# Optimization experiments

Hardware: AMD Instinct MI355X
Metric: run time of the kernel (lower is better)

Reference implementation:

```python
import jax, jax.numpy as jnp
import numpy as np

DIM = 1024
NUM_HEADS = 16
HEAD_DIM = DIM // NUM_HEADS
SCALE = DIM ** (-0.5)  # NOTE: original scales by full dim, not head_dim


def setup_inputs() -> dict:
    key = jax.random.key(0)
    ks = jax.random.split(key, 5)
    B, S = 2, 2048
    x = jax.random.normal(ks[0], (B, S, DIM), dtype=jnp.float32)
    w_qkv = jax.random.normal(ks[1], (DIM, 3 * DIM), dtype=jnp.float32) * (DIM ** -0.5)
    b_qkv = jax.random.normal(ks[2], (3 * DIM,), dtype=jnp.float32) * 0.02
    w_proj = jax.random.normal(ks[3], (DIM, DIM), dtype=jnp.float32) * (DIM ** -0.5)
    b_proj = jax.random.normal(ks[4], (DIM,), dtype=jnp.float32) * 0.02
    return {"x": x, "w_qkv": w_qkv, "b_qkv": b_qkv, "w_proj": w_proj, "b_proj": b_proj}


def reference(x, w_qkv, b_qkv, w_proj, b_proj):
    B, S, D = x.shape
    qkv = x @ w_qkv + b_qkv                                  # [B,S,3D]
    qkv = qkv.reshape(B, S, NUM_HEADS, 3 * HEAD_DIM).transpose(0, 2, 1, 3)  # [B,H,S,3hd]
    q, k, v = jnp.split(qkv, 3, axis=-1)                     # each [B,H,S,hd]
    attn = jnp.einsum("bhqd,bhkd->bhqk", q, k) * SCALE       # [B,H,S,S]
    attn = jax.nn.softmax(attn, axis=-1)
    out = jnp.einsum("bhqk,bhkd->bhqd", attn, v)             # [B,H,S,hd]
    out = out.transpose(0, 2, 1, 3).reshape(B, S, D)
    return out @ w_proj + b_proj
```

## Files before the change

kernel.cpp:

```cpp
#include <hip/hip_runtime.h>
#include <hip/hip_bf16.h>

#define DIM 1024
#define NH 16
#define HD 64
#define BB 2
#define SS 2048
#define MROWS (BB * SS)
#define SCALE 0.03125f
#define SC_LOG2E 0.04508422002778011f

typedef unsigned short u16;
typedef unsigned int u32;
typedef __attribute__((ext_vector_type(8))) short short8;
typedef __attribute__((ext_vector_type(4))) float f32x4;

__device__ __forceinline__ u16 f2bf(float f) {
  union { float f; u32 u; } v; v.f = f;
  return (u16)((v.u + 0x7fffu + ((v.u >> 16) & 1u)) >> 16);
}

__device__ __forceinline__ u32 pack2bf(float a, float b) {
  union { __hip_bfloat162 h; u32 u; } cv;
  cv.h = __float22bfloat162_rn(make_float2(a, b));
  return cv.u;
}

__device__ __forceinline__ void async16(const u16* g, u16* l) {
  __builtin_amdgcn_global_load_lds(
      (const __attribute__((address_space(1))) void*)(const void*)g,
      (__attribute__((address_space(3))) void*)(void*)l, 16, 0, 0);
}

__device__ __forceinline__ short8 ld8(const u16* p) { return *(const short8*)p; }

__global__ void cvt_kernel(const float* __restrict__ in, u16* __restrict__ out, int n4) {
  int i = blockIdx.x * blockDim.x + threadIdx.x;
  if (i < n4) {
    float4 v = ((const float4*)in)[i];
    u32 lo = (u32)f2bf(v.x) | ((u32)f2bf(v.y) << 16);
    u32 hi = (u32)f2bf(v.z) | ((u32)f2bf(v.w) << 16);
    ((uint2*)out)[i] = make_uint2(lo, hi);
  }
}

__global__ void tconv_kernel(const float* __restrict__ in, u16* __restrict__ out, int R, int C) {
  __shared__ u16 t[64 * 65];
  int c0 = blockIdx.x * 64, r0 = blockIdx.y * 64;
  #pragma unroll
  for (int i = 0; i < 16; i++) {
    int j = i * 256 + threadIdx.x;
    int rr = j >> 6, cc = j & 63;
    t[rr * 65 + cc] = f2bf(in[(size_t)(r0 + rr) * C + c0 + cc]);
  }
  __syncthreads();
  #pragma unroll
  for (int i = 0; i < 16; i++) {
    int j = i * 256 + threadIdx.x;
    int oc = j >> 6, orr = j & 63;
    out[(size_t)(c0 + oc) * R + r0 + orr] = t[orr * 65 + oc];
  }
}

template <int MODE>
__global__ __launch_bounds__(256, 2) void gemm_bt(
    const u16* __restrict__ A, const u16* __restrict__ Bt,
    const float* __restrict__ bias, void* __restrict__ C,
    u16* __restrict__ vT, int M, int N, int K) {
  __shared__ __align__(16) u16 As[128 * 32];
  __shared__ __align__(16) u16 Bs[128 * 32];
  const int tid = threadIdx.x;
  const int w = tid >> 6, l = tid & 63;
  const int r = l & 15, q = l >> 4;
  const int m0 = blockIdx.y * 128, n0 = blockIdx.x * 128;
  const int qm = (w & 1) * 64, qn = (w >> 1) * 64;

  const size_t aoff = (size_t)(m0 + w * 16 + (l >> 2)) * K + (size_t)(l & 3) * 8;
  const size_t boff = (size_t)(n0 + w * 16 + (l >> 2)) * K + (size_t)(l & 3) * 8;
  u16* alds = &As[(w * 64 + l) * 8];
  u16* blds = &Bs[(w * 64 + l) * 8];

  f32x4 acc[4][4] = {};
  for (int k0 = 0; k0 < K; k0 += 32) {
    async16(A + aoff + k0, alds);
    async16(A + aoff + (size_t)64 * K + k0, alds + 2048);
    async16(Bt + boff + k0, blds);
    async16(Bt + boff + (size_t)64 * K + k0, blds + 2048);
    __syncthreads();
    short8 af[4], bfr[4];
    #pragma unroll
    for (int i = 0; i < 4; i++) af[i] = ld8(&As[(qm + i * 16 + r) * 32 + q * 8]);
    #pragma unroll
    for (int j = 0; j < 4; j++) bfr[j] = ld8(&Bs[(qn + j * 16 + r) * 32 + q * 8]);
    #pragma unroll
    for (int i = 0; i < 4; i++)
      #pragma unroll
      for (int j = 0; j < 4; j++)
        acc[i][j] = __builtin_amdgcn_mfma_f32_16x16x32_bf16(af[i], bfr[j], acc[i][j], 0, 0, 0);
    __syncthreads();
  }
  #pragma unroll
  for (int i = 0; i < 4; i++) {
    int ro = m0 + qm + i * 16 + q * 4;
    #pragma unroll
    for (int j = 0; j < 4; j++) {
      int col = n0 + qn + j * 16 + r;
      float bv = bias[col];
      float v0 = acc[i][j][0] + bv, v1 = acc[i][j][1] + bv;
      float v2 = acc[i][j][2] + bv, v3 = acc[i][j][3] + bv;
      if (MODE == 1) {
        float* out = (float*)C;
        out[(size_t)(ro + 0) * N + col] = v0;
        out[(size_t)(ro + 1) * N + col] = v1;
        out[(size_t)(ro + 2) * N + col] = v2;
        out[(size_t)(ro + 3) * N + col] = v3;
      } else {
        int h = col / 192, wi = col - h * 192;
        if (wi >= 128) {
          int bb = ro >> 11, s = ro & 2047, d = wi - 128;
          uint2 pk = make_uint2(pack2bf(v0, v1), pack2bf(v2, v3));
          *(uint2*)&vT[((size_t)((bb * NH + h) * HD + d)) * SS + s] = pk;
        } else {
          u16* qk2 = (u16*)C;
          qk2[(size_t)(ro + 0) * 2048 + h * 128 + wi] = f2bf(v0);
          qk2[(size_t)(ro + 1) * 2048 + h * 128 + wi] = f2bf(v1);
          qk2[(size_t)(ro + 2) * 2048 + h * 128 + wi] = f2bf(v2);
          qk2[(size_t)(ro + 3) * 2048 + h * 128 + wi] = f2bf(v3);
        }
      }
    }
  }
}

__global__ __launch_bounds__(256, 2) void attn3_kernel(
    const u16* __restrict__ qk2, const u16* __restrict__ vT,
    u16* __restrict__ attno) {
  __shared__ __align__(16) u16 Ks[128 * 64];
  __shared__ __align__(16) u16 Vs[64 * 128];
  __shared__ __align__(16) u16 pb[4][32 * 136];
  const int tid = threadIdx.x;
  const int w = tid >> 6, l = tid & 63;
  const int r = l & 15, q = l >> 4;
  const int b = blockIdx.z, h = blockIdx.y, q0 = blockIdx.x * 128;

  const u16* qb = qk2 + (size_t)b * SS * 2048;
  const u16* kB = qb + h * 128 + 64;
  const u16* vB = vT + (size_t)((b * NH + h) * HD) * SS;
  u16* pw = &pb[w][0];

  short8 qf[2][2];
  #pragma unroll
  for (int i = 0; i < 2; i++)
    #pragma unroll
    for (int kq = 0; kq < 2; kq++)
      qf[i][kq] = ld8(qb + (size_t)(q0 + w * 32 + i * 16 + r) * 2048 + h * 128 + kq * 32 + q * 8);

  const int klrow = l >> 3;
  const int kchunk = (l & 7) ^ klrow;
  const int vlrow = l >> 4;
  const int vslot = l & 15;

  f32x4 oacc[2][4] = {};
  float lacc[2] = {0.f, 0.f};

  for (int kv0 = 0; kv0 < SS; kv0 += 128) {
    #pragma unroll
    for (int t = 0; t < 4; t++) {
      int sl = (w * 4 + t) * 8 + klrow;
      async16(kB + (size_t)(kv0 + sl) * 2048 + kchunk * 8, &Ks[(w * 4 + t) * 512 + l * 8]);
    }
    #pragma unroll
    for (int t = 0; t < 4; t++) {
      int d = (w * 4 + t) * 4 + vlrow;
      int c = vslot ^ (t * 4 + vlrow);
      async16(vB + (size_t)d * SS + kv0 + c * 8, &Vs[(w * 4 + t) * 512 + l * 8]);
    }
    __syncthreads();

    f32x4 sacc[8][2] = {};
    #pragma unroll
    for (int j = 0; j < 8; j++) {
      int sl = j * 16 + r;
      short8 a0 = ld8(&Ks[sl * 64 + ((q ^ (r & 7)) * 8)]);
      short8 a1 = ld8(&Ks[sl * 64 + (((4 + q) ^ (r & 7)) * 8)]);
      #pragma unroll
      for (int i = 0; i < 2; i++) {
        sacc[j][i] = __builtin_amdgcn_mfma_f32_16x16x32_bf16(a0, qf[i][0], sacc[j][i], 0, 0, 0);
        sacc[j][i] = __builtin_amdgcn_mfma_f32_16x16x32_bf16(a1, qf[i][1], sacc[j][i], 0, 0, 0);
      }
    }
    float rs0 = 0.f, rs1 = 0.f;
    #pragma unroll
    for (int j = 0; j < 8; j++)
      #pragma unroll
      for (int i = 0; i < 2; i++) {
        float p0 = __builtin_exp2f(sacc[j][i][0] * SC_LOG2E);
        float p1 = __builtin_exp2f(sacc[j][i][1] * SC_LOG2E);
        float p2 = __builtin_exp2f(sacc[j][i][2] * SC_LOG2E);
        float p3 = __builtin_exp2f(sacc[j][i][3] * SC_LOG2E);
        if (i == 0) rs0 += (p0 + p1) + (p2 + p3);
        else        rs1 += (p0 + p1) + (p2 + p3);
        uint2 pk = make_uint2(pack2bf(p0, p1), pack2bf(p2, p3));
        *(uint2*)&pw[(i * 16 + r) * 136 + j * 16 + q * 4] = pk;
      }
    rs0 += __shfl_xor(rs0, 16); rs0 += __shfl_xor(rs0, 32);
    rs1 += __shfl_xor(rs1, 16); rs1 += __shfl_xor(rs1, 32);
    lacc[0] += rs0;
    lacc[1] += rs1;
    #pragma unroll
    for (int ks = 0; ks < 4; ks++) {
      short8 pa0 = ld8(&pw[(size_t)r * 136 + ks * 32 + q * 8]);
      short8 pa1 = ld8(&pw[(size_t)(16 + r) * 136 + ks * 32 + q * 8]);
      #pragma unroll
      for (int dj = 0; dj < 4; dj++) {
        short8 vb = ld8(&Vs[(dj * 16 + r) * 128 + (((ks * 4 + q) ^ r) * 8)]);
        oacc[0][dj] = __builtin_amdgcn_mfma_f32_16x16x32_bf16(pa0, vb, oacc[0][dj], 0, 0, 0);
        oacc[1][dj] = __builtin_amdgcn_mfma_f32_16x16x32_bf16(pa1, vb, oacc[1][dj], 0, 0, 0);
      }
    }
    __syncthreads();
  }
  #pragma unroll
  for (int i = 0; i < 2; i++)
    #pragma unroll
    for (int e = 0; e < 4; e++) {
      float dn = __shfl(lacc[i], q * 4 + e, 16);
      float di = 1.f / dn;
      int row = q0 + w * 32 + i * 16 + q * 4 + e;
      #pragma unroll
      for (int dj = 0; dj < 4; dj++)
        attno[(size_t)(b * SS + row) * DIM + h * HD + dj * 16 + r] =
            f2bf(oacc[i][dj][e] * di);
    }
}

extern "C" void kernel_launch(void* const* d_in, const int* in_sizes, int n_in,
                              void* d_out, int out_size, void* d_ws, size_t ws_size,
                              hipStream_t stream) {
  const float* x      = (const float*)d_in[0];
  const float* w_qkv  = (const float*)d_in[1];
  const float* b_qkv  = (const float*)d_in[2];
  const float* w_proj = (const float*)d_in[3];
  const float* b_proj = (const float*)d_in[4];
  float* out = (float*)d_out;
  char* ws = (char*)d_ws;
  u16* xb     = (u16*)(ws);
  u16* wqkvT  = (u16*)(ws + ((size_t)8  << 20));
  u16* wprojT = (u16*)(ws + ((size_t)14 << 20));
  u16* qk2    = (u16*)(ws + ((size_t)16 << 20));
  u16* attno  = (u16*)(ws + ((size_t)32 << 20));
  u16* vT     = (u16*)(ws + ((size_t)40 << 20));

  cvt_kernel<<<4096, 256, 0, stream>>>(x, xb, MROWS * DIM / 4);
  tconv_kernel<<<dim3(48, 16), 256, 0, stream>>>(w_qkv, wqkvT, DIM, 3 * DIM);
  tconv_kernel<<<dim3(16, 16), 256, 0, stream>>>(w_proj, wprojT, DIM, DIM);
  gemm_bt<0><<<dim3(24, 32), 256, 0, stream>>>(xb, wqkvT, b_qkv, qk2, vT, MROWS, 3 * DIM, DIM);
  attn3_kernel<<<dim3(16, NH, BB), 256, 0, stream>>>(qk2, vT, attno);
  gemm_bt<1><<<dim3(8, 32), 256, 0, stream>>>(attno, wprojT, b_proj, out, nullptr, MROWS, DIM, DIM);
}
```

Measured before the change: 215.3 us.

## Fold softmax scale into Q, compute row sums via MFMA, halve attention query tile

```diff
diff --git a/kernel.cpp b/kernel.cpp
--- a/kernel.cpp
+++ b/kernel.cpp
@@ -7,7 +7,6 @@
 #define BB 2
 #define SS 2048
 #define MROWS (BB * SS)
-#define SCALE 0.03125f
 #define SC_LOG2E 0.04508422002778011f
 
 typedef unsigned short u16;
@@ -121,6 +120,7 @@
           uint2 pk = make_uint2(pack2bf(v0, v1), pack2bf(v2, v3));
           *(uint2*)&vT[((size_t)((bb * NH + h) * HD + d)) * SS + s] = pk;
         } else {
+          if (wi < 64) { v0 *= SC_LOG2E; v1 *= SC_LOG2E; v2 *= SC_LOG2E; v3 *= SC_LOG2E; }
           u16* qk2 = (u16*)C;
           qk2[(size_t)(ro + 0) * 2048 + h * 128 + wi] = f2bf(v0);
           qk2[(size_t)(ro + 1) * 2048 + h * 128 + wi] = f2bf(v1);
@@ -132,36 +132,38 @@
   }
 }
 
-__global__ __launch_bounds__(256, 2) void attn3_kernel(
+__global__ __launch_bounds__(256, 3) void attn4_kernel(
     const u16* __restrict__ qk2, const u16* __restrict__ vT,
     u16* __restrict__ attno) {
   __shared__ __align__(16) u16 Ks[128 * 64];
   __shared__ __align__(16) u16 Vs[64 * 128];
-  __shared__ __align__(16) u16 pb[4][32 * 136];
+  __shared__ __align__(16) u16 pb[4][16 * 136];
   const int tid = threadIdx.x;
   const int w = tid >> 6, l = tid & 63;
   const int r = l & 15, q = l >> 4;
-  const int b = blockIdx.z, h = blockIdx.y, q0 = blockIdx.x * 128;
+  const int b = blockIdx.z, h = blockIdx.y, q0 = blockIdx.x * 64;
 
   const u16* qb = qk2 + (size_t)b * SS * 2048;
   const u16* kB = qb + h * 128 + 64;
   const u16* vB = vT + (size_t)((b * NH + h) * HD) * SS;
   u16* pw = &pb[w][0];
 
-  short8 qf[2][2];
-  #pragma unroll
-  for (int i = 0; i < 2; i++)
-    #pragma unroll
-    for (int kq = 0; kq < 2; kq++)
-      qf[i][kq] = ld8(qb + (size_t)(q0 + w * 32 + i * 16 + r) * 2048 + h * 128 + kq * 32 + q * 8);
+  short8 qf[2];
+  #pragma unroll
+  for (int kq = 0; kq < 2; kq++)
+    qf[kq] = ld8(qb + (size_t)(q0 + w * 16 + r) * 2048 + h * 128 + kq * 32 + q * 8);
+
+  short8 ones;
+  #pragma unroll
+  for (int e = 0; e < 8; e++) ones[e] = (short)0x3F80;
 
   const int klrow = l >> 3;
   const int kchunk = (l & 7) ^ klrow;
   const int vlrow = l >> 4;
   const int vslot = l & 15;
 
-  f32x4 oacc[2][4] = {};
-  float lacc[2] = {0.f, 0.f};
+  f32x4 oacc[4] = {};
+  f32x4 dacc = {};
 
   for (int kv0 = 0; kv0 < SS; kv0 += 128) {
     #pragma unroll
@@ -177,61 +179,45 @@
     }
     __syncthreads();
 
-    f32x4 sacc[8][2] = {};
+    f32x4 sacc[8] = {};
     #pragma unroll
     for (int j = 0; j < 8; j++) {
       int sl = j * 16 + r;
       short8 a0 = ld8(&Ks[sl * 64 + ((q ^ (r & 7)) * 8)]);
       short8 a1 = ld8(&Ks[sl * 64 + (((4 + q) ^ (r & 7)) * 8)]);
-      #pragma unroll
-      for (int i = 0; i < 2; i++) {
-        sacc[j][i] = __builtin_amdgcn_mfma_f32_16x16x32_bf16(a0, qf[i][0], sacc[j][i], 0, 0, 0);
-        sacc[j][i] = __builtin_amdgcn_mfma_f32_16x16x32_bf16(a1, qf[i][1], sacc[j][i], 0, 0, 0);
-      }
-    }
-    float rs0 = 0.f, rs1 = 0.f;
-    #pragma unroll
-    for (int j = 0; j < 8; j++)
-      #pragma unroll
-      for (int i = 0; i < 2; i++) {
-        float p0 = __builtin_exp2f(sacc[j][i][0] * SC_LOG2E);
-        float p1 = __builtin_exp2f(sacc[j][i][1] * SC_LOG2E);
-        float p2 = __builtin_exp2f(sacc[j][i][2] * SC_LOG2E);
-        float p3 = __builtin_exp2f(sacc[j][i][3] * SC_LOG2E);
-        if (i == 0) rs0 += (p0 + p1) + (p2 + p3);
-        else        rs1 += (p0 + p1) + (p2 + p3);
-        uint2 pk = make_uint2(pack2bf(p0, p1), pack2bf(p2, p3));
-        *(uint2*)&pw[(i * 16 + r) * 136 + j * 16 + q * 4] = pk;
-      }
-    rs0 += __shfl_xor(rs0, 16); rs0 += __shfl_xor(rs0, 32);
-    rs1 += __shfl_xor(rs1, 16); rs1 += __shfl_xor(rs1, 32);
-    lacc[0] += rs0;
-    lacc[1] += rs1;
+      sacc[j] = __builtin_amdgcn_mfma_f32_16x16x32_bf16(a0, qf[0], sacc[j], 0, 0, 0);
+      sacc[j] = __builtin_amdgcn_mfma_f32_16x16x32_bf16(a1, qf[1], sacc[j], 0, 0, 0);
+    }
+    #pragma unroll
+    for (int j = 0; j < 8; j++) {
+      float p0 = __builtin_exp2f(sacc[j][0]);
+      float p1 = __builtin_exp2f(sacc[j][1]);
+      float p2 = __builtin_exp2f(sacc[j][2]);
+      float p3 = __builtin_exp2f(sacc[j][3]);
+      uint2 pk = make_uint2(pack2bf(p0, p1), pack2bf(p2, p3));
+      *(uint2*)&pw[r * 136 + j * 16 + q * 4] = pk;
+    }
     #pragma unroll
     for (int ks = 0; ks < 4; ks++) {
-      short8 pa0 = ld8(&pw[(size_t)r * 136 + ks * 32 + q * 8]);
-      short8 pa1 = ld8(&pw[(size_t)(16 + r) * 136 + ks * 32 + q * 8]);
+      short8 pa = ld8(&pw[r * 136 + ks * 32 + q * 8]);
+      dacc = __builtin_amdgcn_mfma_f32_16x16x32_bf16(pa, ones, dacc, 0, 0, 0);
       #pragma unroll
       for (int dj = 0; dj < 4; dj++) {
         short8 vb = ld8(&Vs[(dj * 16 + r) * 128 + (((ks * 4 + q) ^ r) * 8)]);
-        oacc[0][dj] = __builtin_amdgcn_mfma_f32_16x16x32_bf16(pa0, vb, oacc[0][dj], 0, 0, 0);
-        oacc[1][dj] = __builtin_amdgcn_mfma_f32_16x16x32_bf16(pa1, vb, oacc[1][dj], 0, 0, 0);
+        oacc[dj] = __builtin_amdgcn_mfma_f32_16x16x32_bf16(pa, vb, oacc[dj], 0, 0, 0);
       }
     }
     __syncthreads();
   }
   #pragma unroll
-  for (int i = 0; i < 2; i++)
-    #pragma unroll
-    for (int e = 0; e < 4; e++) {
-      float dn = __shfl(lacc[i], q * 4 + e, 16);
-      float di = 1.f / dn;
-      int row = q0 + w * 32 + i * 16 + q * 4 + e;
-      #pragma unroll
-      for (int dj = 0; dj < 4; dj++)
-        attno[(size_t)(b * SS + row) * DIM + h * HD + dj * 16 + r] =
-            f2bf(oacc[i][dj][e] * di);
-    }
+  for (int e = 0; e < 4; e++) {
+    float di = 1.f / dacc[e];
+    int row = q0 + w * 16 + q * 4 + e;
+    #pragma unroll
+    for (int dj = 0; dj < 4; dj++)
+      attno[(size_t)(b * SS + row) * DIM + h * HD + dj * 16 + r] =
+          f2bf(oacc[dj][e] * di);
+  }
 }
 
 extern "C" void kernel_launch(void* const* d_in, const int* in_sizes, int n_in,
@@ -255,6 +241,6 @@
   tconv_kernel<<<dim3(48, 16), 256, 0, stream>>>(w_qkv, wqkvT, DIM, 3 * DIM);
   tconv_kernel<<<dim3(16, 16), 256, 0, stream>>>(w_proj, wprojT, DIM, DIM);
   gemm_bt<0><<<dim3(24, 32), 256, 0, stream>>>(xb, wqkvT, b_qkv, qk2, vT, MROWS, 3 * DIM, DIM);
-  attn3_kernel<<<dim3(16, NH, BB), 256, 0, stream>>>(qk2, vT, attno);
+  attn4_kernel<<<dim3(32, NH, BB), 256, 0, stream>>>(qk2, vT, attno);
   gemm_bt<1><<<dim3(8, 32), 256, 0, stream>>>(attno, wprojT, b_proj, out, nullptr, MROWS, DIM, DIM);
 }
```

New measurement: 215.7 us. No clear change (+0.1%).
